# Optimization experiments

Hardware: AMD Instinct MI355X
Metric: run time of the kernel (lower is better)

## Reference

```python
import jax, jax.numpy as jnp
import numpy as np

ALPHA = 0.5
NUM_NB = 8


def setup_inputs() -> dict:
    key = jax.random.key(0)
    k1, k2 = jax.random.split(key)
    pc1 = jax.random.normal(k1, (4, 3, 8192), dtype=jnp.float32)
    pred_flow = jax.random.normal(k2, (4, 3, 8192), dtype=jnp.float32)
    return {"pc1": pc1, "pred_flow": pred_flow}


def reference(pc1, pred_flow):
    # pc1, pred_flow: [B, 3, N] -> [B, N, 3]
    B, _, N = pc1.shape
    k = NUM_NB
    p = jnp.transpose(pc1, (0, 2, 1))         # [B, N, 3]
    f = jnp.transpose(pred_flow, (0, 2, 1))   # [B, N, 3]

    sq = jnp.sum(p * p, axis=-1)
    sqrdist = sq[:, :, None] + sq[:, None, :] - 2.0 * jnp.einsum('bnd,bmd->bnm', p, p)

    # k+1 smallest (sorted ascending), drop self (first column)
    neg_d, kidx = jax.lax.top_k(-sqrdist, k + 1)  # descending in -d == ascending in d
    dists = -neg_d[:, :, 1:]                      # [B, N, k]
    kidx = kidx[:, :, 1:]                         # [B, N, k]
    dists = jnp.maximum(dists, 0.0)

    # softmax over all N*k weights per batch
    w = jax.nn.softmax(jnp.exp(-dists / ALPHA).reshape(B, N * k), axis=1)
    w = w.reshape(B, N, k)

    # gather neighbor flows: [B, N, k, 3]
    grouped = jnp.take_along_axis(f[:, None, :, :],
                                  kidx[:, :, :, None],
                                  axis=2)
    diff = jnp.linalg.norm(grouped - f[:, :, None, :], axis=3)  # [B, N, k]
    diff_flow = (N * w * diff).sum(axis=2)                      # [B, N]
    return jnp.mean(diff_flow)
```

## Files before the change

kernel.cpp:

```cpp
#include <hip/hip_runtime.h>
#include <math.h>

#define BATCH 4
#define NQ 8192
#define KNB 8
#define K1 9
#define NB 512
#define XMIN -4.5f
#define XSCALE (NB / 9.0f)
#define CAP 34
#define THW 512
#define THS 128
#define SPART 2
#define IDXMASK 8191u
#define KEYMASK 0xFFFFE000u
#define EPS_S 1e-3f

static __device__ __forceinline__ int binOf(float x) {
  return min(max((int)((x - XMIN) * XSCALE), 0), NB - 1);
}

#define CHAIN9(KEY) { unsigned kk = (KEY); \
  _Pragma("unroll") \
  for (int j = 0; j < K1; ++j) { \
    unsigned lo = min(kk, nk[j]); unsigned hi = max(kk, nk[j]); \
    nk[j] = lo; kk = hi; } }

#define CHAIN8(KEY) { unsigned kk = (KEY); \
  _Pragma("unroll") \
  for (int j = 0; j < KNB; ++j) { \
    unsigned lo = min(kk, nk[j]); unsigned hi = max(kk, nk[j]); \
    nk[j] = lo; kk = hi; } }

#define DRAINS() { \
  for (int ii = 0; ii < cnt; ++ii) { \
    int j = sbuf[base + ii]; \
    float dx = qx - sxs[bq + j], dy = qy - sys[bq + j], dz = qz - szs[bq + j]; \
    float d = dx*dx + dy*dy + dz*dz; \
    unsigned key = (__float_as_uint(d) & KEYMASK) | ssi[bq + j]; \
    if (key < nk[K1-1]) CHAIN9(key); \
  } \
  cnt = 0; \
  if (nk[K1-1] != 0xFFFFFFFFu) { \
    float td = __uint_as_float(nk[K1-1] | 0x1FFFu); \
    thetaS = fminf(thetaS, 0.5f*(td - qq) + EPS_S); \
  } }

#define GPROC(SS, JLOCAL) { \
  if ((SS) <= thetaS) { sbuf[base + cnt] = (unsigned short)(JLOCAL); cnt++; } }

#define SCORE4(S0,S1,S2,S3, X,Y,Z,H) \
  float S0 = fmaf(nqx, X.x, fmaf(nqy, Y.x, fmaf(nqz, Z.x, H.x))); \
  float S1 = fmaf(nqx, X.y, fmaf(nqy, Y.y, fmaf(nqz, Z.y, H.y))); \
  float S2 = fmaf(nqx, X.z, fmaf(nqy, Y.z, fmaf(nqz, Z.z, H.z))); \
  float S3 = fmaf(nqx, X.w, fmaf(nqy, Y.w, fmaf(nqz, Z.w, H.w)));

#define BURST(CB) { \
  const int jb = (CB) << 4; \
  const int ti = (bq + jb) >> 2; \
  const float4 X0=x4[ti],X1=x4[ti+1],X2=x4[ti+2],X3=x4[ti+3]; \
  const float4 Y0=y4[ti],Y1=y4[ti+1],Y2=y4[ti+2],Y3=y4[ti+3]; \
  const float4 Z0=z4[ti],Z1=z4[ti+1],Z2=z4[ti+2],Z3=z4[ti+3]; \
  const float4 H0=h4[ti],H1=h4[ti+1],H2=h4[ti+2],H3=h4[ti+3]; \
  SCORE4(s0,s1,s2,s3, X0,Y0,Z0,H0); \
  SCORE4(s4,s5,s6,s7, X1,Y1,Z1,H1); \
  SCORE4(s8,s9,sa,sb, X2,Y2,Z2,H2); \
  SCORE4(sc,sd,se,sf, X3,Y3,Z3,H3); \
  GPROC(s0,jb+0); GPROC(s1,jb+1); GPROC(s2,jb+2); GPROC(s3,jb+3); \
  GPROC(s4,jb+4); GPROC(s5,jb+5); GPROC(s6,jb+6); GPROC(s7,jb+7); \
  GPROC(s8,jb+8); GPROC(s9,jb+9); GPROC(sa,jb+10); GPROC(sb,jb+11); \
  GPROC(sc,jb+12); GPROC(sd,jb+13); GPROC(se,jb+14); GPROC(sf,jb+15); }

__global__ __launch_bounds__(1024) void sort_kernel(
    const float* __restrict__ pc,
    float* __restrict__ sxs, float* __restrict__ sys, float* __restrict__ szs,
    float* __restrict__ shs, unsigned* __restrict__ ssi,
    unsigned* __restrict__ binStart)
{
  __shared__ unsigned h[NB];
  __shared__ unsigned hs[NB];
  const int b = blockIdx.x;
  const int tid = threadIdx.x;
  const float* __restrict__ px = pc + (size_t)b * 3 * NQ;
  const float* __restrict__ py = px + NQ;
  const float* __restrict__ pz = px + 2 * NQ;
  if (tid < NB) h[tid] = 0u;
  __syncthreads();
#pragma unroll
  for (int k = 0; k < NQ / 1024; ++k) {
    const int n = tid + k * 1024;
    atomicAdd(&h[binOf(px[n])], 1u);
  }
  __syncthreads();
  if (tid < NB) hs[tid] = h[tid];
  __syncthreads();
  for (int off = 1; off < NB; off <<= 1) {
    unsigned v = (tid < NB && tid >= off) ? hs[tid - off] : 0u;
    __syncthreads();
    if (tid < NB) hs[tid] += v;
    __syncthreads();
  }
  if (tid < NB) {
    const unsigned excl = hs[tid] - h[tid];
    binStart[b * (NB + 1) + tid] = excl;
    h[tid] = excl;
  }
  if (tid == 0) binStart[b * (NB + 1) + NB] = NQ;
  __syncthreads();
  const int bq = b * NQ;
#pragma unroll
  for (int k = 0; k < NQ / 1024; ++k) {
    const int n = tid + k * 1024;
    const float x = px[n], y = py[n], z = pz[n];
    const unsigned pos = atomicAdd(&h[binOf(x)], 1u);
    const int o = bq + (int)pos;
    sxs[o] = x; sys[o] = y; szs[o] = z;
    shs[o] = 0.5f * (x * x + y * y + z * z);
    ssi[o] = (unsigned)n;
  }
}

__global__ __launch_bounds__(256) void theta_kernel(
    const float* __restrict__ sxs, const float* __restrict__ sys,
    const float* __restrict__ szs, unsigned* __restrict__ thetaOut)
{
  __shared__ float swx[THW], swy[THW], swz[THW];
  const int b = blockIdx.y, p = blockIdx.z;
  const int B0 = blockIdx.x * 256;
  const int bq = b * NQ;
  const int stg0 = min(max(B0 - 128, 0), NQ - THW);
#pragma unroll
  for (int k = 0; k < THW / 256; ++k) {
    const int i = threadIdx.x + k * 256;
    swx[i] = sxs[bq + stg0 + i];
    swy[i] = sys[bq + stg0 + i];
    swz[i] = szs[bq + stg0 + i];
  }
  __syncthreads();
  const int s = B0 + threadIdx.x;
  const float qx = swx[s - stg0], qy = swy[s - stg0], qz = swz[s - stg0];
  const int w = min(max(s - 128, stg0), stg0 + THW - 256) - stg0;
  unsigned nk[K1];
#pragma unroll
  for (int j = 0; j < K1; ++j) nk[j] = 0xFFFFFFFFu;
  for (int k = 0; k < THS; ++k) {
    const int i = w + 2 * k + p;
    const float dx = qx - swx[i], dy = qy - swy[i], dz = qz - swz[i];
    const float d = dx * dx + dy * dy + dz * dz;
    CHAIN9(__float_as_uint(d));
  }
  thetaOut[(size_t)(bq + s) * SPART + p] = nk[K1 - 1] | 0x1FFFu;
}

__global__ __launch_bounds__(256) void knn_kernel(
    const float* __restrict__ sxs, const float* __restrict__ sys,
    const float* __restrict__ szs, const float* __restrict__ shs,
    const unsigned* __restrict__ ssi, const unsigned* __restrict__ binStart,
    const unsigned* __restrict__ thetaIn, unsigned* __restrict__ wsK, int P)
{
  __shared__ unsigned short sbuf[256 * CAP];
  const int b = blockIdx.y, p = blockIdx.z;
  const int s = blockIdx.x * 256 + threadIdx.x;
  const int bq = b * NQ;
  const float qx = sxs[bq + s], qy = sys[bq + s], qz = szs[bq + s];
  const float nqx = -qx, nqy = -qy, nqz = -qz;
  const float qq = qx * qx + qy * qy + qz * qz;

  const uint2 th = ((const uint2*)thetaIn)[bq + s];
  const float thetaD = __uint_as_float(min(th.x, th.y));
  float thetaS = 0.5f * (thetaD - qq) + EPS_S;
  const float r = sqrtf(thetaD) * 1.0001f + 1e-7f;
  unsigned LO = binStart[b * (NB + 1) + binOf(qx - r)];
  unsigned HI = binStart[b * (NB + 1) + binOf(qx + r) + 1];
  for (int off = 32; off; off >>= 1) {
    LO = min(LO, (unsigned)__shfl_xor((int)LO, off));
    HI = max(HI, (unsigned)__shfl_xor((int)HI, off));
  }
  const int b0 = __builtin_amdgcn_readfirstlane((int)LO) >> 4;
  const int b1 = (__builtin_amdgcn_readfirstlane((int)HI) + 15) >> 4;
  const int nb = b1 - b0;
  const int st = b0 + (p * nb) / P;
  const int en = b0 + ((p + 1) * nb) / P;

  unsigned nk[K1];
#pragma unroll
  for (int j = 0; j < K1; ++j) nk[j] = 0xFFFFFFFFu;
  const unsigned base = (unsigned)threadIdx.x * CAP;
  int cnt = 0;
  const float4* __restrict__ x4 = (const float4*)sxs;
  const float4* __restrict__ y4 = (const float4*)sys;
  const float4* __restrict__ z4 = (const float4*)szs;
  const float4* __restrict__ h4 = (const float4*)shs;

  for (int cb = st; cb < en; ++cb) {
    if (__any(cnt >= CAP - 16)) { DRAINS(); }
    BURST(cb);
  }
  DRAINS();

#pragma unroll
  for (int j = 0; j < K1; ++j)
    wsK[((size_t)(b * P + p) * K1 + j) * NQ + s] = nk[j];
}

__global__ __launch_bounds__(64) void loss_kernel(
    const float* __restrict__ pc, const float* __restrict__ pf,
    const float* __restrict__ sxs, const float* __restrict__ sys,
    const float* __restrict__ szs, const unsigned* __restrict__ ssi,
    const unsigned* __restrict__ wsK, float* __restrict__ acc,
    unsigned* __restrict__ doneCtr, float* __restrict__ out,
    int P, int nBlocks)
{
  const int b = blockIdx.y;
  const int s = blockIdx.x * 64 + threadIdx.x;
  const int bq = b * NQ;
  const float* __restrict__ px = pc + (size_t)b * 3 * NQ;
  const float* __restrict__ py = px + NQ;
  const float* __restrict__ pz = px + 2 * NQ;
  const float* __restrict__ fx = pf + (size_t)b * 3 * NQ;
  const float* __restrict__ fy = fx + NQ;
  const float* __restrict__ fz = fx + 2 * NQ;

  const unsigned qorig = ssi[bq + s];
  unsigned nk[KNB];
#pragma unroll
  for (int j = 0; j < KNB; ++j) nk[j] = 0xFFFFFFFFu;

  const int total = P * K1;
  const size_t stride0 = (size_t)b * P * K1;
  for (int m0 = 0; m0 < total; m0 += K1) {
    unsigned kb[K1];
#pragma unroll
    for (int u = 0; u < K1; ++u)
      kb[u] = wsK[(stride0 + m0 + u) * NQ + s];
#pragma unroll
    for (int u = 0; u < K1; ++u) {
      unsigned key = kb[u];
      if ((key & IDXMASK) == qorig) continue;
      if (key < nk[KNB - 1]) CHAIN8(key);
    }
  }

  const float qx = sxs[bq + s], qy = sys[bq + s], qz = szs[bq + s];
  const float fqx = fx[qorig], fqy = fy[qorig], fqz = fz[qorig];
  float ssum = 0.f, sdsum = 0.f;
#pragma unroll
  for (int j = 0; j < KNB; ++j) {
    const int i = (int)(nk[j] & IDXMASK);
    const float dx = qx - px[i], dy = qy - py[i], dz = qz - pz[i];
    const float d = dx * dx + dy * dy + dz * dz;
    const float e = expf(expf(-2.0f * d));
    const float gx = fx[i] - fqx, gy = fy[i] - fqy, gz = fz[i] - fqz;
    const float diff = sqrtf(gx * gx + gy * gy + gz * gz);
    ssum += e; sdsum += e * diff;
  }

  for (int off = 32; off > 0; off >>= 1) {
    ssum += __shfl_down(ssum, off);
    sdsum += __shfl_down(sdsum, off);
  }
  if (threadIdx.x == 0) {
    atomicAdd(&acc[b * 2 + 0], ssum);
    atomicAdd(&acc[b * 2 + 1], sdsum);
    __threadfence();
    const unsigned done = atomicAdd(doneCtr, 1u);
    if (done == (unsigned)(nBlocks - 1)) {
      float sT = 0.f;
      for (int bb = 0; bb < BATCH; ++bb) {
        const float se = atomicAdd(&acc[bb * 2 + 0], 0.f);
        const float sd = atomicAdd(&acc[bb * 2 + 1], 0.f);
        sT += sd / se;
      }
      out[0] = sT * (1.0f / BATCH);
    }
  }
}

extern "C" void kernel_launch(void* const* d_in, const int* in_sizes, int n_in,
                              void* d_out, int out_size, void* d_ws, size_t ws_size,
                              hipStream_t stream) {
  const float* pc = (const float*)d_in[0];
  const float* pf = (const float*)d_in[1];
  float* out = (float*)d_out;

  char* w = (char*)d_ws;
  float*    acc      = (float*)w;
  unsigned* doneCtr  = (unsigned*)(w + 64);
  unsigned* binStart = (unsigned*)(w + 256);
  const size_t SA = 16384;
  float*    sxs = (float*)(w + SA);
  float*    sys = (float*)(w + SA + 1 * 131072);
  float*    szs = (float*)(w + SA + 2 * 131072);
  float*    shs = (float*)(w + SA + 3 * 131072);
  unsigned* ssi = (unsigned*)(w + SA + 4 * 131072);
  const size_t TH = SA + 5 * 131072;
  unsigned* thetaBuf = (unsigned*)(w + TH);
  const size_t WK = TH + (size_t)BATCH * NQ * SPART * 4;
  unsigned* wsK = (unsigned*)(w + WK);

  const size_t needP16 = WK + (size_t)BATCH * NQ * 16 * K1 * 4;
  const size_t needP8  = WK + (size_t)BATCH * NQ * 8  * K1 * 4;
  const size_t needP4  = WK + (size_t)BATCH * NQ * 4  * K1 * 4;
  const int P = (ws_size >= needP16) ? 16 : (ws_size >= needP8) ? 8
              : (ws_size >= needP4) ? 4 : 2;

  hipMemsetAsync(d_ws, 0, 128, stream);

  sort_kernel<<<dim3(BATCH), 1024, 0, stream>>>(pc, sxs, sys, szs, shs, ssi,
                                                binStart);
  theta_kernel<<<dim3(NQ / 256, BATCH, SPART), 256, 0, stream>>>(
      sxs, sys, szs, thetaBuf);
  knn_kernel<<<dim3(NQ / 256, BATCH, P), 256, 0, stream>>>(
      sxs, sys, szs, shs, ssi, binStart, thetaBuf, wsK, P);
  const int nBlocks = (NQ / 64) * BATCH;
  loss_kernel<<<dim3(NQ / 64, BATCH), 64, 0, stream>>>(
      pc, pf, sxs, sys, szs, ssi, wsK, acc, doneCtr, out, P, nBlocks);
}
```

Baseline: 140.4 us.

## Split sort into parallel hist/prefix/scatter kernels and store full keys in candidate buffer

The single-block-per-batch sort kernel is replaced by three grid-wide kernels (global histogram via atomics, single-block prefix scan, parallel scatter), so the binning stage uses many CUs instead of four. In the KNN kernel, candidates now store a packed distance|index key computed from the already-available score, plus the original index loaded as uint4 alongside coordinates. This removes the gather and distance recompute in the drain loop. CAP shrinks to 21 because the buffer entries are now 32-bit, and P becomes a template parameter. The cost is two extra kernel launches, a larger memset, an extra index stream per burst, and more frequent drains. Scatter order within bins now depends on global atomics and is nondeterministic.

```diff
diff --git a/kernel.cpp b/kernel.cpp
--- a/kernel.cpp
+++ b/kernel.cpp
@@ -8,7 +8,7 @@
 #define NB 512
 #define XMIN -4.5f
 #define XSCALE (NB / 9.0f)
-#define CAP 34
+#define CAP 21
 #define THW 512
 #define THS 128
 #define SPART 2
@@ -34,20 +34,17 @@
 
 #define DRAINS() { \
   for (int ii = 0; ii < cnt; ++ii) { \
-    int j = sbuf[base + ii]; \
-    float dx = qx - sxs[bq + j], dy = qy - sys[bq + j], dz = qz - szs[bq + j]; \
-    float d = dx*dx + dy*dy + dz*dz; \
-    unsigned key = (__float_as_uint(d) & KEYMASK) | ssi[bq + j]; \
+    const unsigned key = sbuf[base + ii]; \
     if (key < nk[K1-1]) CHAIN9(key); \
   } \
   cnt = 0; \
-  if (nk[K1-1] != 0xFFFFFFFFu) { \
-    float td = __uint_as_float(nk[K1-1] | 0x1FFFu); \
-    thetaS = fminf(thetaS, 0.5f*(td - qq) + EPS_S); \
-  } }
-
-#define GPROC(SS, JLOCAL) { \
-  if ((SS) <= thetaS) { sbuf[base + cnt] = (unsigned short)(JLOCAL); cnt++; } }
+  { const float td = __uint_as_float(nk[K1-1] | 0x1FFFu); \
+    thetaS = fminf(thetaS, 0.5f*(td - qq) + EPS_S); } }
+
+#define GPROC(SS, OI) { \
+  if ((SS) <= thetaS) { \
+    const float dd = fmaxf(fmaf(2.0f, (SS), qq), 0.0f); \
+    sbuf[base + cnt] = (__float_as_uint(dd) & KEYMASK) | (OI); cnt++; } }
 
 #define SCORE4(S0,S1,S2,S3, X,Y,Z,H) \
   float S0 = fmaf(nqx, X.x, fmaf(nqy, Y.x, fmaf(nqz, Z.x, H.x))); \
@@ -62,62 +59,61 @@
   const float4 Y0=y4[ti],Y1=y4[ti+1],Y2=y4[ti+2],Y3=y4[ti+3]; \
   const float4 Z0=z4[ti],Z1=z4[ti+1],Z2=z4[ti+2],Z3=z4[ti+3]; \
   const float4 H0=h4[ti],H1=h4[ti+1],H2=h4[ti+2],H3=h4[ti+3]; \
+  const uint4  I0=i4[ti],I1=i4[ti+1],I2=i4[ti+2],I3=i4[ti+3]; \
   SCORE4(s0,s1,s2,s3, X0,Y0,Z0,H0); \
   SCORE4(s4,s5,s6,s7, X1,Y1,Z1,H1); \
   SCORE4(s8,s9,sa,sb, X2,Y2,Z2,H2); \
   SCORE4(sc,sd,se,sf, X3,Y3,Z3,H3); \
-  GPROC(s0,jb+0); GPROC(s1,jb+1); GPROC(s2,jb+2); GPROC(s3,jb+3); \
-  GPROC(s4,jb+4); GPROC(s5,jb+5); GPROC(s6,jb+6); GPROC(s7,jb+7); \
-  GPROC(s8,jb+8); GPROC(s9,jb+9); GPROC(sa,jb+10); GPROC(sb,jb+11); \
-  GPROC(sc,jb+12); GPROC(sd,jb+13); GPROC(se,jb+14); GPROC(sf,jb+15); }
-
-__global__ __launch_bounds__(1024) void sort_kernel(
-    const float* __restrict__ pc,
+  GPROC(s0,I0.x); GPROC(s1,I0.y); GPROC(s2,I0.z); GPROC(s3,I0.w); \
+  GPROC(s4,I1.x); GPROC(s5,I1.y); GPROC(s6,I1.z); GPROC(s7,I1.w); \
+  GPROC(s8,I2.x); GPROC(s9,I2.y); GPROC(sa,I2.z); GPROC(sb,I2.w); \
+  GPROC(sc,I3.x); GPROC(sd,I3.y); GPROC(se,I3.z); GPROC(sf,I3.w); }
+
+__global__ __launch_bounds__(256) void hist_kernel(
+    const float* __restrict__ pc, unsigned* __restrict__ hist)
+{
+  const int t = blockIdx.x * 256 + threadIdx.x;
+  const int b = t >> 13, n = t & (NQ - 1);
+  atomicAdd(&hist[b * NB + binOf(pc[(size_t)b * 3 * NQ + n])], 1u);
+}
+
+__global__ __launch_bounds__(512) void prefix_kernel(
+    unsigned* __restrict__ hist, unsigned* __restrict__ binStart)
+{
+  __shared__ unsigned sc[NB];
+  const int t = threadIdx.x;
+  for (int b = 0; b < BATCH; ++b) {
+    const unsigned c = hist[b * NB + t];
+    sc[t] = c;
+    __syncthreads();
+    for (int o = 1; o < NB; o <<= 1) {
+      unsigned a = (t >= o) ? sc[t - o] : 0u;
+      __syncthreads();
+      sc[t] += a;
+      __syncthreads();
+    }
+    const unsigned excl = sc[t] - c;
+    binStart[b * (NB + 1) + t] = excl;
+    hist[b * NB + t] = excl;
+    if (t == NB - 1) binStart[b * (NB + 1) + NB] = NQ;
+    __syncthreads();
+  }
+}
+
+__global__ __launch_bounds__(256) void scatter_kernel(
+    const float* __restrict__ pc, unsigned* __restrict__ cursor,
     float* __restrict__ sxs, float* __restrict__ sys, float* __restrict__ szs,
-    float* __restrict__ shs, unsigned* __restrict__ ssi,
-    unsigned* __restrict__ binStart)
-{
-  __shared__ unsigned h[NB];
-  __shared__ unsigned hs[NB];
-  const int b = blockIdx.x;
-  const int tid = threadIdx.x;
+    float* __restrict__ shs, unsigned* __restrict__ ssi)
+{
+  const int t = blockIdx.x * 256 + threadIdx.x;
+  const int b = t >> 13, n = t & (NQ - 1);
   const float* __restrict__ px = pc + (size_t)b * 3 * NQ;
-  const float* __restrict__ py = px + NQ;
-  const float* __restrict__ pz = px + 2 * NQ;
-  if (tid < NB) h[tid] = 0u;
-  __syncthreads();
-#pragma unroll
-  for (int k = 0; k < NQ / 1024; ++k) {
-    const int n = tid + k * 1024;
-    atomicAdd(&h[binOf(px[n])], 1u);
-  }
-  __syncthreads();
-  if (tid < NB) hs[tid] = h[tid];
-  __syncthreads();
-  for (int off = 1; off < NB; off <<= 1) {
-    unsigned v = (tid < NB && tid >= off) ? hs[tid - off] : 0u;
-    __syncthreads();
-    if (tid < NB) hs[tid] += v;
-    __syncthreads();
-  }
-  if (tid < NB) {
-    const unsigned excl = hs[tid] - h[tid];
-    binStart[b * (NB + 1) + tid] = excl;
-    h[tid] = excl;
-  }
-  if (tid == 0) binStart[b * (NB + 1) + NB] = NQ;
-  __syncthreads();
-  const int bq = b * NQ;
-#pragma unroll
-  for (int k = 0; k < NQ / 1024; ++k) {
-    const int n = tid + k * 1024;
-    const float x = px[n], y = py[n], z = pz[n];
-    const unsigned pos = atomicAdd(&h[binOf(x)], 1u);
-    const int o = bq + (int)pos;
-    sxs[o] = x; sys[o] = y; szs[o] = z;
-    shs[o] = 0.5f * (x * x + y * y + z * z);
-    ssi[o] = (unsigned)n;
-  }
+  const float x = px[n], y = px[NQ + n], z = px[2 * NQ + n];
+  const unsigned pos = atomicAdd(&cursor[b * NB + binOf(x)], 1u);
+  const int o = b * NQ + (int)pos;
+  sxs[o] = x; sys[o] = y; szs[o] = z;
+  shs[o] = 0.5f * (x * x + y * y + z * z);
+  ssi[o] = (unsigned)n;
 }
 
 __global__ __launch_bounds__(256) void theta_kernel(
@@ -152,13 +148,14 @@
   thetaOut[(size_t)(bq + s) * SPART + p] = nk[K1 - 1] | 0x1FFFu;
 }
 
+template<int P>
 __global__ __launch_bounds__(256) void knn_kernel(
     const float* __restrict__ sxs, const float* __restrict__ sys,
     const float* __restrict__ szs, const float* __restrict__ shs,
     const unsigned* __restrict__ ssi, const unsigned* __restrict__ binStart,
-    const unsigned* __restrict__ thetaIn, unsigned* __restrict__ wsK, int P)
-{
-  __shared__ unsigned short sbuf[256 * CAP];
+    const unsigned* __restrict__ thetaIn, unsigned* __restrict__ wsK)
+{
+  __shared__ unsigned sbuf[256 * CAP];
   const int b = blockIdx.y, p = blockIdx.z;
   const int s = blockIdx.x * 256 + threadIdx.x;
   const int bq = b * NQ;
@@ -191,6 +188,7 @@
   const float4* __restrict__ y4 = (const float4*)sys;
   const float4* __restrict__ z4 = (const float4*)szs;
   const float4* __restrict__ h4 = (const float4*)shs;
+  const uint4*  __restrict__ i4 = (const uint4*)ssi;
 
   for (int cb = st; cb < en; ++cb) {
     if (__any(cnt >= CAP - 16)) { DRAINS(); }
@@ -235,7 +233,7 @@
       kb[u] = wsK[(stride0 + m0 + u) * NQ + s];
 #pragma unroll
     for (int u = 0; u < K1; ++u) {
-      unsigned key = kb[u];
+      const unsigned key = kb[u];
       if ((key & IDXMASK) == qorig) continue;
       if (key < nk[KNB - 1]) CHAIN8(key);
     }
@@ -286,8 +284,9 @@
   char* w = (char*)d_ws;
   float*    acc      = (float*)w;
   unsigned* doneCtr  = (unsigned*)(w + 64);
-  unsigned* binStart = (unsigned*)(w + 256);
-  const size_t SA = 16384;
+  unsigned* hist     = (unsigned*)(w + 256);
+  unsigned* binStart = (unsigned*)(w + 8448);
+  const size_t SA = 16896;
   float*    sxs = (float*)(w + SA);
   float*    sys = (float*)(w + SA + 1 * 131072);
   float*    szs = (float*)(w + SA + 2 * 131072);
@@ -300,18 +299,25 @@
 
   const size_t needP16 = WK + (size_t)BATCH * NQ * 16 * K1 * 4;
   const size_t needP8  = WK + (size_t)BATCH * NQ * 8  * K1 * 4;
-  const size_t needP4  = WK + (size_t)BATCH * NQ * 4  * K1 * 4;
-  const int P = (ws_size >= needP16) ? 16 : (ws_size >= needP8) ? 8
-              : (ws_size >= needP4) ? 4 : 2;
-
-  hipMemsetAsync(d_ws, 0, 128, stream);
-
-  sort_kernel<<<dim3(BATCH), 1024, 0, stream>>>(pc, sxs, sys, szs, shs, ssi,
-                                                binStart);
+  const int P = (ws_size >= needP16) ? 16 : (ws_size >= needP8) ? 8 : 4;
+
+  hipMemsetAsync(d_ws, 0, 8448, stream);
+
+  hist_kernel<<<dim3(BATCH * NQ / 256), 256, 0, stream>>>(pc, hist);
+  prefix_kernel<<<dim3(1), 512, 0, stream>>>(hist, binStart);
+  scatter_kernel<<<dim3(BATCH * NQ / 256), 256, 0, stream>>>(
+      pc, hist, sxs, sys, szs, shs, ssi);
   theta_kernel<<<dim3(NQ / 256, BATCH, SPART), 256, 0, stream>>>(
       sxs, sys, szs, thetaBuf);
-  knn_kernel<<<dim3(NQ / 256, BATCH, P), 256, 0, stream>>>(
-      sxs, sys, szs, shs, ssi, binStart, thetaBuf, wsK, P);
+  if (P == 16)
+    knn_kernel<16><<<dim3(NQ / 256, BATCH, 16), 256, 0, stream>>>(
+        sxs, sys, szs, shs, ssi, binStart, thetaBuf, wsK);
+  else if (P == 8)
+    knn_kernel<8><<<dim3(NQ / 256, BATCH, 8), 256, 0, stream>>>(
+        sxs, sys, szs, shs, ssi, binStart, thetaBuf, wsK);
+  else
+    knn_kernel<4><<<dim3(NQ / 256, BATCH, 4), 256, 0, stream>>>(
+        sxs, sys, szs, shs, ssi, binStart, thetaBuf, wsK);
   const int nBlocks = (NQ / 64) * BATCH;
   loss_kernel<<<dim3(NQ / 64, BATCH), 64, 0, stream>>>(
       pc, pf, sxs, sys, szs, ssi, wsK, acc, doneCtr, out, P, nBlocks);
```

Result: slower. 144.1 us (+2.6%).
